# Kernel tuning notes

Measured on AMD Instinct MI355X. Metric: run time of the kernel, lower is better.

The kernel has to match this reference:

```python
import jax, jax.numpy as jnp
import numpy as np

B, S, D, H = 4, 2048, 1024, 16
DH = D // H  # head dim = 64
MASK_VALUE = -1000000.0


def setup_inputs() -> dict:
    key = jax.random.key(0)
    ks = jax.random.split(key, 8)
    return {
        "key": jax.random.normal(ks[0], (B, S, D), jnp.float32),
        "query": jax.random.normal(ks[1], (B, S, D), jnp.float32),
        "value": jax.random.normal(ks[2], (B, S, D), jnp.float32),
        "valid_lens": jax.random.randint(ks[3], (B,), 0, 2048, jnp.int32),
        # nn.Linear weights stored as [out_features, in_features]
        "Wk": jax.random.normal(ks[4], (D, D), jnp.float32) / np.sqrt(D),
        "Wq": jax.random.normal(ks[5], (D, D), jnp.float32) / np.sqrt(D),
        "Wv": jax.random.normal(ks[6], (D, D), jnp.float32) / np.sqrt(D),
        "Wo": jax.random.normal(ks[7], (D, D), jnp.float32) / np.sqrt(D),
    }


def _split_heads(x):
    # [B, S, D] -> [B, H, S, DH]
    return x.reshape(B, S, H, DH).transpose(0, 2, 1, 3)


def reference(key, query, value, valid_lens, Wk, Wq, Wv, Wo):
    # projections (Linear: x @ W^T, bias=False)
    q = _split_heads(query @ Wq.T)  # [B, H, S, DH]
    k = _split_heads(key @ Wk.T)
    v = _split_heads(value @ Wv.T)

    scale = 1.0 / jnp.sqrt(jnp.asarray(DH, q.dtype))
    scores = jnp.einsum("bhqd,bhkd->bhqk", q, k) * scale  # [B, H, S, S]

    # valid_lens masks the key axis per batch element (same for all heads/queries)
    key_mask = jnp.arange(S) < valid_lens[:, None]  # [B, S]
    scores = jnp.where(key_mask[:, None, None, :], scores, MASK_VALUE)

    attn = jax.nn.softmax(scores, axis=-1)
    out = jnp.einsum("bhqk,bhkd->bhqd", attn, v)  # [B, H, S, DH]
    out = out.transpose(0, 2, 1, 3).reshape(B, S, D)  # concat heads
    return out @ Wo.T
```

## Files before the change

### kernel.cpp

```cpp
#include <hip/hip_runtime.h>
#include <hip/hip_bf16.h>
#include <stdint.h>

typedef __bf16 bf16;
typedef __bf16 bf16x4 __attribute__((ext_vector_type(4)));
typedef __bf16 bf16x8 __attribute__((ext_vector_type(8)));
typedef float f32x4 __attribute__((ext_vector_type(4)));
typedef float f32x8 __attribute__((ext_vector_type(8)));

#define MFMA16 __builtin_amdgcn_mfma_f32_16x16x32_bf16

__device__ __forceinline__ void gload_lds16(void* lds, const void* g) {
  __builtin_amdgcn_global_load_lds(
      (const __attribute__((address_space(1))) unsigned int*)g,
      (__attribute__((address_space(3))) unsigned int*)lds, 16, 0, 0);
}

#define S_BARRIER() __builtin_amdgcn_s_barrier()
#define WAIT_LGKM0()                                   \
  do {                                                 \
    asm volatile("s_waitcnt lgkmcnt(0)" ::: "memory"); \
    __builtin_amdgcn_sched_barrier(0);                 \
  } while (0)
#define WAIT_VM(n) asm volatile("s_waitcnt vmcnt(" #n ")" ::: "memory")

__global__ __launch_bounds__(256) void cvt3(
    const float* __restrict__ s0, const float* __restrict__ s1,
    const float* __restrict__ s2, bf16* __restrict__ d0,
    bf16* __restrict__ d1, bf16* __restrict__ d2) {
  const float* srcs[3] = {s0, s1, s2};
  bf16* dsts[3] = {d0, d1, d2};
  const float* src = srcs[blockIdx.y];
  bf16* dst = dsts[blockIdx.y];
  int i = (blockIdx.x * 256 + threadIdx.x) * 4;
  f32x4 v = *(const f32x4*)(src + i);
  bf16x4 o;
#pragma unroll
  for (int j = 0; j < 4; j++) o[j] = (bf16)v[j];
  *(bf16x4*)(dst + i) = o;
}

__global__ __launch_bounds__(256) void cvt1(const float* __restrict__ src,
                                            bf16* __restrict__ dst) {
  int i = (blockIdx.x * 256 + threadIdx.x) * 4;
  f32x4 v = *(const f32x4*)(src + i);
  bf16x4 o;
#pragma unroll
  for (int j = 0; j < 4; j++) o[j] = (bf16)v[j];
  *(bf16x4*)(dst + i) = o;
}

__global__ __launch_bounds__(256) void cvt4(const float* __restrict__ w0,
                                            const float* __restrict__ w1,
                                            const float* __restrict__ w2,
                                            const float* __restrict__ w3,
                                            bf16* __restrict__ dst) {
  const float* srcs[4] = {w0, w1, w2, w3};
  const float* src = srcs[blockIdx.y];
  int i = (blockIdx.x * 256 + threadIdx.x) * 4;
  f32x4 v = *(const f32x4*)(src + i);
  bf16x4 o;
#pragma unroll
  for (int j = 0; j < 4; j++) o[j] = (bf16)v[j];
  *(bf16x4*)(dst + (size_t)blockIdx.y * 1048576 + i) = o;
}

__device__ __forceinline__ void gemmF_body(const bf16* __restrict__ A,
                                           const bf16* __restrict__ W,
                                           void* __restrict__ Craw, int mode,
                                           int m0, int n0, bf16* smem) {
  constexpr int K = 1024;
  const int t = threadIdx.x;
  const int lane = t & 63;
  const int m16 = lane & 15;
  const int quad = (lane >> 4) & 3;
  const int sw = m16 & 7;
  const int w = t >> 6;
  const int wm = (w >> 2) * 64;
  const int wn = (w & 3) * 64;

  const bf16* Ab = A + (size_t)m0 * K;
  const bf16* Bb = W + (size_t)n0 * K;

  auto STG = [&](int buf, int kt) {
    bf16* dA = smem + buf * 24576;
    bf16* dB = dA + 8192;
    const bf16* sA = Ab + kt * 64;
    const bf16* sB = Bb + kt * 64;
#pragma unroll
    for (int ld = 0; ld < 2; ld++) {
      int idx = ld * 512 + t;
      int row = idx >> 3;
      int c = (idx & 7) ^ (row & 7);
      gload_lds16(dA + idx * 8, sA + (size_t)row * K + c * 8);
    }
#pragma unroll
    for (int ld = 0; ld < 4; ld++) {
      int idx = ld * 512 + t;
      int row = idx >> 3;
      int c = (idx & 7) ^ (row & 7);
      gload_lds16(dB + idx * 8, sB + (size_t)row * K + c * 8);
    }
  };

  bf16x8 aR[8], bR[8];
  auto LD = [&](int buf) {
    const bf16* As = smem + buf * 24576;
    const bf16* Bs = As + 8192;
#pragma unroll
    for (int f = 0; f < 4; f++)
#pragma unroll
      for (int ks = 0; ks < 2; ks++) {
        aR[f * 2 + ks] = *(const bf16x8*)&As[(wm + f * 16 + m16) * 64 +
                                             (((ks * 4 + quad) ^ sw) * 8)];
        bR[f * 2 + ks] = *(const bf16x8*)&Bs[(wn + f * 16 + m16) * 64 +
                                             (((ks * 4 + quad) ^ sw) * 8)];
      }
  };

  f32x4 acc[4][4];
#pragma unroll
  for (int f = 0; f < 4; f++)
#pragma unroll
    for (int g = 0; g < 4; g++) acc[f][g] = (f32x4){0.f, 0.f, 0.f, 0.f};

  auto MM = [&]() {
    __builtin_amdgcn_s_setprio(1);
#pragma unroll
    for (int f = 0; f < 4; f++)
#pragma unroll
      for (int g = 0; g < 4; g++)
#pragma unroll
        for (int ks = 0; ks < 2; ks++)
          acc[f][g] = MFMA16(aR[f * 2 + ks], bR[g * 2 + ks], acc[f][g], 0, 0, 0);
    __builtin_amdgcn_s_setprio(0);
  };

  STG(0, 0);
  STG(1, 1);
  WAIT_VM(6);
  S_BARRIER();

  int bufR = 0;
#pragma unroll 1
  for (int kt = 0; kt < 14; ++kt) {
    LD(bufR);
    int bufS = bufR + 2;
    if (bufS >= 3) bufS -= 3;
    STG(bufS, kt + 2);
    S_BARRIER();
    WAIT_LGKM0();
    MM();
    WAIT_VM(6);
    S_BARRIER();
    bufR = (bufR + 1 == 3) ? 0 : bufR + 1;
  }
  LD(bufR);
  S_BARRIER();
  WAIT_LGKM0();
  MM();
  WAIT_VM(0);
  S_BARRIER();
  bufR = (bufR + 1 == 3) ? 0 : bufR + 1;
  LD(bufR);
  S_BARRIER();
  WAIT_LGKM0();
  MM();

#pragma unroll
  for (int f = 0; f < 4; f++) {
    int rbase = m0 + wm + f * 16 + quad * 4;
#pragma unroll
    for (int g = 0; g < 4; g++) {
      int col = n0 + wn + g * 16 + m16;
#pragma unroll
      for (int r = 0; r < 4; r++) {
        int row = rbase + r;
        if (mode == 0) {
          ((float*)Craw)[(size_t)row * 1024 + col] = acc[f][g][r];
        } else {
          int b = row >> 11, s = row & 2047;
          int h = col >> 6, d = col & 63;
          bf16 v = (bf16)acc[f][g][r];
          if (mode == 1)
            ((bf16*)Craw)[(((size_t)(b * 16 + h)) * 2048 + s) * 64 + d] = v;
          else
            ((bf16*)Craw)[(((size_t)(b * 16 + h)) * 64 + d) * 2048 + s] = v;
        }
      }
    }
  }
}

__global__ __launch_bounds__(512, 2) void gemm_qkv(
    const bf16* __restrict__ xq, const bf16* __restrict__ xk,
    const bf16* __restrict__ xv, const bf16* __restrict__ wb,
    const int* __restrict__ vlen, bf16* __restrict__ qp,
    bf16* __restrict__ kp, bf16* __restrict__ vt) {
  __shared__ bf16 smem[73728];
  const int m0 = blockIdx.y * 128;
  const int n0 = blockIdx.x * 256;
  const int z = blockIdx.z;
  if (z >= 1) {
    int b = m0 >> 11;
    int s0 = m0 & 2047;
    int vl = vlen[b];
    if (vl != 0 && s0 >= vl) return;
  }
  const bf16* A = (z == 0) ? xq : (z == 1) ? xk : xv;
  const bf16* W = wb + (size_t)z * 1048576;
  bf16* C = (z == 0) ? qp : (z == 1) ? kp : vt;
  gemmF_body(A, W, C, (z == 2) ? 2 : 1, m0, n0, smem);
}

__global__ __launch_bounds__(512, 2) void gemm_one(const bf16* __restrict__ A,
                                                   const bf16* __restrict__ W,
                                                   void* __restrict__ Craw,
                                                   int mode) {
  __shared__ bf16 smem[73728];
  gemmF_body(A, W, Craw, mode, blockIdx.y * 128, blockIdx.x * 256, smem);
}

template <int AF32, int WF32>
__global__ __launch_bounds__(256) void gemm_bt(const void* __restrict__ Araw,
                                               const void* __restrict__ Wraw,
                                               void* __restrict__ Craw,
                                               int mode) {
  constexpr int K = 1024;
  __shared__ bf16 As[128 * 32];
  __shared__ bf16 Bs[128 * 32];
  const int t = threadIdx.x;
  const int lane = t & 63;
  const int quad = lane >> 4;
  const int m16 = lane & 15;
  const int w = t >> 6;
  const int m0 = blockIdx.y * 128;
  const int n0 = blockIdx.x * 128;
  const int wm = (w >> 1) * 64;
  const int wn = (w & 1) * 64;

  f32x4 acc[4][4];
#pragma unroll
  for (int i = 0; i < 4; i++)
#pragma unroll
    for (int j = 0; j < 4; j++) acc[i][j] = (f32x4){0.f, 0.f, 0.f, 0.f};

  for (int kt = 0; kt < K / 32; kt++) {
    bf16x8 aR[2], bR[2];
#pragma unroll
    for (int p = 0; p < 2; p++) {
      int idx = p * 256 + t;
      int row = idx >> 2;
      int ce = (idx & 3) * 8;
      size_t aoff = (size_t)(m0 + row) * K + kt * 32 + ce;
      size_t boff = (size_t)(n0 + row) * K + kt * 32 + ce;
      if constexpr (AF32) {
        f32x8 av = *(const f32x8*)((const float*)Araw + aoff);
#pragma unroll
        for (int j = 0; j < 8; j++) aR[p][j] = (bf16)av[j];
      } else {
        aR[p] = *(const bf16x8*)((const bf16*)Araw + aoff);
      }
      if constexpr (WF32) {
        f32x8 bv = *(const f32x8*)((const float*)Wraw + boff);
#pragma unroll
        for (int j = 0; j < 8; j++) bR[p][j] = (bf16)bv[j];
      } else {
        bR[p] = *(const bf16x8*)((const bf16*)Wraw + boff);
      }
    }
    __syncthreads();
#pragma unroll
    for (int p = 0; p < 2; p++) {
      int idx = p * 256 + t;
      *(bf16x8*)&As[idx * 8] = aR[p];
      *(bf16x8*)&Bs[idx * 8] = bR[p];
    }
    __syncthreads();

    bf16x8 af[4], bfr[4];
#pragma unroll
    for (int i = 0; i < 4; i++) {
      af[i] = *(const bf16x8*)&As[(wm + i * 16 + m16) * 32 + quad * 8];
      bfr[i] = *(const bf16x8*)&Bs[(wn + i * 16 + m16) * 32 + quad * 8];
    }
#pragma unroll
    for (int i = 0; i < 4; i++)
#pragma unroll
      for (int j = 0; j < 4; j++)
        acc[i][j] = MFMA16(af[i], bfr[j], acc[i][j], 0, 0, 0);
  }

#pragma unroll
  for (int i = 0; i < 4; i++) {
    int rbase = m0 + wm + i * 16 + quad * 4;
#pragma unroll
    for (int j = 0; j < 4; j++) {
      int col = n0 + wn + j * 16 + m16;
#pragma unroll
      for (int r = 0; r < 4; r++) {
        int row = rbase + r;
        if (mode == 0) {
          ((float*)Craw)[(size_t)row * 1024 + col] = acc[i][j][r];
        } else {
          int b = row >> 11, s = row & 2047;
          int h = col >> 6, d = col & 63;
          bf16 v = (bf16)acc[i][j][r];
          if (mode == 1)
            ((bf16*)Craw)[(((size_t)(b * 16 + h)) * 2048 + s) * 64 + d] = v;
          else
            ((bf16*)Craw)[(((size_t)(b * 16 + h)) * 64 + d) * 2048 + s] = v;
        }
      }
    }
  }
}

__global__ __launch_bounds__(256) void attn(const bf16* __restrict__ qp,
                                            const bf16* __restrict__ kp,
                                            const bf16* __restrict__ vt,
                                            const int* __restrict__ vlen,
                                            bf16* __restrict__ ctx) {
  __shared__ bf16 Ks[64 * 64];
  __shared__ bf16 Vs[64 * 64];
  __shared__ bf16 Ps[4 * 32 * 72];

  const int t = threadIdx.x;
  const int lane = t & 63;
  const int quad = lane >> 4;
  const int m16 = lane & 15;
  const int sw = m16 & 7;
  const int w = t >> 6;
  const int bh = blockIdx.y;
  const int qt = blockIdx.x;
  const int b = bh >> 4;
  const int h = bh & 15;
  const int vl = vlen[b];

  const float C1 = 0.18033688f;
  const float C2 = 46.166241f;
  const float mArg = (vl == 0) ? 0.0f : -12800.0f;

  bf16x8 qf[2][2];
#pragma unroll
  for (int a = 0; a < 2; a++) {
    const bf16* qb =
        qp + ((size_t)(bh * 2048 + qt * 128 + w * 32 + a * 16 + m16)) * 64;
    qf[a][0] = *(const bf16x8*)(qb + quad * 8);
    qf[a][1] = *(const bf16x8*)(qb + 32 + quad * 8);
  }

  float rsum[2][4] = {{0.f, 0.f, 0.f, 0.f}, {0.f, 0.f, 0.f, 0.f}};
  f32x4 o[2][4];
#pragma unroll
  for (int a = 0; a < 2; a++)
#pragma unroll
    for (int nt = 0; nt < 4; nt++) o[a][nt] = (f32x4){0.f, 0.f, 0.f, 0.f};

  const int ktEnd = (vl == 0) ? 32 : ((vl + 63) >> 6);

  for (int kt = 0; kt < ktEnd; kt++) {
    __syncthreads();
#pragma unroll
    for (int p = 0; p < 2; p++) {
      int idx = p * 256 + t;
      int row = idx >> 3;
      int gc = (idx & 7) ^ (row & 7);
      gload_lds16(&Ks[idx * 8],
                  &kp[((size_t)(bh * 2048 + kt * 64 + row)) * 64 + gc * 8]);
      gload_lds16(&Vs[idx * 8],
                  &vt[((size_t)(bh * 64 + row)) * 2048 + kt * 64 + gc * 8]);
    }
    __syncthreads();

    f32x4 s[2][4];
#pragma unroll
    for (int a = 0; a < 2; a++)
#pragma unroll
      for (int nt = 0; nt < 4; nt++) s[a][nt] = (f32x4){0.f, 0.f, 0.f, 0.f};
#pragma unroll
    for (int nt = 0; nt < 4; nt++) {
      int key = nt * 16 + m16;
#pragma unroll
      for (int ks = 0; ks < 2; ks++) {
        bf16x8 kf =
            *(const bf16x8*)&Ks[key * 64 + (((ks * 4 + quad) ^ sw) * 8)];
        s[0][nt] = MFMA16(qf[0][ks], kf, s[0][nt], 0, 0, 0);
        s[1][nt] = MFMA16(qf[1][ks], kf, s[1][nt], 0, 0, 0);
      }
    }

#pragma unroll
    for (int nt = 0; nt < 4; nt++) {
      bool masked = (kt * 64 + nt * 16 + m16) >= vl;
#pragma unroll
      for (int a = 0; a < 2; a++)
#pragma unroll
        for (int r = 0; r < 4; r++) {
          float arg = masked ? mArg : (s[a][nt][r] * C1 - C2);
          bf16 pb = (bf16)__builtin_amdgcn_exp2f(arg);
          rsum[a][r] += (float)pb;
          Ps[w * 2304 + (a * 16 + quad * 4 + r) * 72 + nt * 16 + m16] = pb;
        }
    }

#pragma unroll
    for (int ks = 0; ks < 2; ks++) {
      bf16x8 pf0 = *(const bf16x8*)&Ps[w * 2304 + m16 * 72 + ks * 32 + quad * 8];
      bf16x8 pf1 =
          *(const bf16x8*)&Ps[w * 2304 + (16 + m16) * 72 + ks * 32 + quad * 8];
#pragma unroll
      for (int nt = 0; nt < 4; nt++) {
        int dh = nt * 16 + m16;
        bf16x8 vf =
            *(const bf16x8*)&Vs[dh * 64 + (((ks * 4 + quad) ^ sw) * 8)];
        o[0][nt] = MFMA16(pf0, vf, o[0][nt], 0, 0, 0);
        o[1][nt] = MFMA16(pf1, vf, o[1][nt], 0, 0, 0);
      }
    }
  }

#pragma unroll
  for (int off = 1; off < 16; off <<= 1)
#pragma unroll
    for (int a = 0; a < 2; a++)
#pragma unroll
      for (int r = 0; r < 4; r++) rsum[a][r] += __shfl_xor(rsum[a][r], off);
#pragma unroll
  for (int a = 0; a < 2; a++)
#pragma unroll
    for (int r = 0; r < 4; r++) rsum[a][r] = 1.0f / rsum[a][r];

#pragma unroll
  for (int a = 0; a < 2; a++)
#pragma unroll
    for (int nt = 0; nt < 4; nt++) {
      int dh = nt * 16 + m16;
#pragma unroll
      for (int r = 0; r < 4; r++) {
        int srow = qt * 128 + w * 32 + a * 16 + quad * 4 + r;
        ctx[((size_t)(b * 2048 + srow)) * 1024 + h * 64 + dh] =
            (bf16)(o[a][nt][r] * rsum[a][r]);
      }
    }
}

extern "C" void kernel_launch(void* const* d_in, const int* in_sizes, int n_in,
                              void* d_out, int out_size, void* d_ws,
                              size_t ws_size, hipStream_t stream) {
  const float* key = (const float*)d_in[0];
  const float* query = (const float*)d_in[1];
  const float* value = (const float*)d_in[2];
  const int* vlen = (const int*)d_in[3];
  const float* Wk = (const float*)d_in[4];
  const float* Wq = (const float*)d_in[5];
  const float* Wv = (const float*)d_in[6];
  const float* Wo = (const float*)d_in[7];

  const size_t NE = (size_t)4 * 2048 * 1024;
  const size_t WE = 1048576;

  const size_t needA = (6 * NE + 4 * WE) * sizeof(bf16);
  const size_t needB = (5 * NE + 4 * WE) * sizeof(bf16);
  dim3 gg(4, 64), gb(512), cb(256);

  if (ws_size >= needA) {
    bf16* qp = (bf16*)d_ws;
    bf16* kp = qp + NE;
    bf16* vt = kp + NE;
    bf16* xq = vt + NE;
    bf16* xk = xq + NE;
    bf16* xv = xk + NE;
    bf16* wb = xv + NE;
    bf16* ctx = xq;

    cvt4<<<dim3(1024, 4), cb, 0, stream>>>(Wq, Wk, Wv, Wo, wb);
    cvt3<<<dim3(8192, 3), cb, 0, stream>>>(query, key, value, xq, xk, xv);
    gemm_qkv<<<dim3(4, 64, 3), gb, 0, stream>>>(xq, xk, xv, wb, vlen, qp, kp,
                                                vt);
    attn<<<dim3(16, 64), cb, 0, stream>>>(qp, kp, vt, vlen, ctx);
    gemm_one<<<gg, gb, 0, stream>>>(ctx, wb + 3 * WE, d_out, 0);
  } else if (ws_size >= needB) {
    bf16* qp = (bf16*)d_ws;
    bf16* kp = qp + NE;
    bf16* vt = kp + NE;
    bf16* ctx = vt + NE;
    bf16* xb = ctx + NE;
    bf16* wb = xb + NE;

    cvt4<<<dim3(1024, 4), cb, 0, stream>>>(Wq, Wk, Wv, Wo, wb);
    cvt1<<<8192, cb, 0, stream>>>(query, xb);
    gemm_one<<<gg, gb, 0, stream>>>(xb, wb + 0 * WE, qp, 1);
    cvt1<<<8192, cb, 0, stream>>>(key, xb);
    gemm_one<<<gg, gb, 0, stream>>>(xb, wb + 1 * WE, kp, 1);
    cvt1<<<8192, cb, 0, stream>>>(value, xb);
    gemm_one<<<gg, gb, 0, stream>>>(xb, wb + 2 * WE, vt, 2);
    attn<<<dim3(16, 64), cb, 0, stream>>>(qp, kp, vt, vlen, ctx);
    gemm_one<<<gg, gb, 0, stream>>>(ctx, wb + 3 * WE, d_out, 0);
  } else {
    bf16* qp = (bf16*)d_ws;
    bf16* kp = qp + NE;
    bf16* vt = kp + NE;
    bf16* ctx = vt + NE;
    dim3 g8(8, 64), b256(256);
    gemm_bt<1, 1><<<g8, b256, 0, stream>>>(query, Wq, qp, 1);
    gemm_bt<1, 1><<<g8, b256, 0, stream>>>(key, Wk, kp, 1);
    gemm_bt<1, 1><<<g8, b256, 0, stream>>>(value, Wv, vt, 2);
    attn<<<dim3(16, 64), b256, 0, stream>>>(qp, kp, vt, vlen, ctx);
    gemm_bt<0, 1><<<g8, b256, 0, stream>>>(ctx, Wo, d_out, 0);
  }
}
```

Before: 320.7 us.

## Double-buffer K/V tiles in attention with 512-thread blocks and XCD-aware mapping

The attention kernel now uses 512-thread blocks covering 256 queries, so each staged K/V tile is reused by twice as many warps. K/V tiles are double-buffered in LDS, with the next tile's async global-to-LDS load issued before computing on the current one, and waits use vmcnt plus raw barriers. Block IDs are remapped so that query tiles of the same head land on the same XCD for L2 reuse. The cost is more LDS per block and fewer blocks in flight, and the raw barrier and vmcnt synchronisation is easy to get wrong.

```diff
diff --git a/kernel.cpp b/kernel.cpp
--- a/kernel.cpp
+++ b/kernel.cpp
@@ -316,23 +316,26 @@
   }
 }
 
-__global__ __launch_bounds__(256) void attn(const bf16* __restrict__ qp,
-                                            const bf16* __restrict__ kp,
-                                            const bf16* __restrict__ vt,
-                                            const int* __restrict__ vlen,
-                                            bf16* __restrict__ ctx) {
-  __shared__ bf16 Ks[64 * 64];
-  __shared__ bf16 Vs[64 * 64];
-  __shared__ bf16 Ps[4 * 32 * 72];
+__global__ __launch_bounds__(512, 4) void attn(const bf16* __restrict__ qp,
+                                               const bf16* __restrict__ kp,
+                                               const bf16* __restrict__ vt,
+                                               const int* __restrict__ vlen,
+                                               bf16* __restrict__ ctx) {
+  __shared__ bf16 Ks[2][4096];
+  __shared__ bf16 Vs[2][4096];
+  __shared__ bf16 Ps[8 * 2304];
 
   const int t = threadIdx.x;
   const int lane = t & 63;
-  const int quad = lane >> 4;
+  const int quad = (lane >> 4) & 3;
   const int m16 = lane & 15;
   const int sw = m16 & 7;
   const int w = t >> 6;
-  const int bh = blockIdx.y;
-  const int qt = blockIdx.x;
+  const int id = blockIdx.y * 8 + blockIdx.x;
+  const int xcd = id & 7;
+  const int j = id >> 3;
+  const int bh = (j >> 3) * 8 + xcd;
+  const int qt = j & 7;
   const int b = bh >> 4;
   const int h = bh & 15;
   const int vl = vlen[b];
@@ -345,7 +348,7 @@
 #pragma unroll
   for (int a = 0; a < 2; a++) {
     const bf16* qb =
-        qp + ((size_t)(bh * 2048 + qt * 128 + w * 32 + a * 16 + m16)) * 64;
+        qp + ((size_t)(bh * 2048 + qt * 256 + w * 32 + a * 16 + m16)) * 64;
     qf[a][0] = *(const bf16x8*)(qb + quad * 8);
     qf[a][1] = *(const bf16x8*)(qb + 32 + quad * 8);
   }
@@ -359,19 +362,28 @@
 
   const int ktEnd = (vl == 0) ? 32 : ((vl + 63) >> 6);
 
+  const int srow = t >> 3;
+  const int sgc = (t & 7) ^ (srow & 7);
+  auto STAGE = [&](int buf, int kt) {
+    gload_lds16(&Ks[buf][t * 8],
+                &kp[((size_t)(bh * 2048 + kt * 64 + srow)) * 64 + sgc * 8]);
+    gload_lds16(&Vs[buf][t * 8],
+                &vt[((size_t)(bh * 64 + srow)) * 2048 + kt * 64 + sgc * 8]);
+  };
+
+  STAGE(0, 0);
+
   for (int kt = 0; kt < ktEnd; kt++) {
-    __syncthreads();
-#pragma unroll
-    for (int p = 0; p < 2; p++) {
-      int idx = p * 256 + t;
-      int row = idx >> 3;
-      int gc = (idx & 7) ^ (row & 7);
-      gload_lds16(&Ks[idx * 8],
-                  &kp[((size_t)(bh * 2048 + kt * 64 + row)) * 64 + gc * 8]);
-      gload_lds16(&Vs[idx * 8],
-                  &vt[((size_t)(bh * 64 + row)) * 2048 + kt * 64 + gc * 8]);
-    }
-    __syncthreads();
+    const int cur = kt & 1;
+    if (kt + 1 < ktEnd) {
+      STAGE(cur ^ 1, kt + 1);
+      WAIT_VM(2);
+    } else {
+      WAIT_VM(0);
+    }
+    S_BARRIER();
+    const bf16* Ksb = Ks[cur];
+    const bf16* Vsb = Vs[cur];
 
     f32x4 s[2][4];
 #pragma unroll
@@ -384,7 +396,7 @@
 #pragma unroll
       for (int ks = 0; ks < 2; ks++) {
         bf16x8 kf =
-            *(const bf16x8*)&Ks[key * 64 + (((ks * 4 + quad) ^ sw) * 8)];
+            *(const bf16x8*)&Ksb[key * 64 + (((ks * 4 + quad) ^ sw) * 8)];
         s[0][nt] = MFMA16(qf[0][ks], kf, s[0][nt], 0, 0, 0);
         s[1][nt] = MFMA16(qf[1][ks], kf, s[1][nt], 0, 0, 0);
       }
@@ -413,11 +425,12 @@
       for (int nt = 0; nt < 4; nt++) {
         int dh = nt * 16 + m16;
         bf16x8 vf =
-            *(const bf16x8*)&Vs[dh * 64 + (((ks * 4 + quad) ^ sw) * 8)];
+            *(const bf16x8*)&Vsb[dh * 64 + (((ks * 4 + quad) ^ sw) * 8)];
         o[0][nt] = MFMA16(pf0, vf, o[0][nt], 0, 0, 0);
         o[1][nt] = MFMA16(pf1, vf, o[1][nt], 0, 0, 0);
       }
     }
+    S_BARRIER();
   }
 
 #pragma unroll
@@ -438,8 +451,8 @@
       int dh = nt * 16 + m16;
 #pragma unroll
       for (int r = 0; r < 4; r++) {
-        int srow = qt * 128 + w * 32 + a * 16 + quad * 4 + r;
-        ctx[((size_t)(b * 2048 + srow)) * 1024 + h * 64 + dh] =
+        int sr = qt * 256 + w * 32 + a * 16 + quad * 4 + r;
+        ctx[((size_t)(b * 2048 + sr)) * 1024 + h * 64 + dh] =
             (bf16)(o[a][nt][r] * rsum[a][r]);
       }
     }
@@ -462,7 +475,7 @@
 
   const size_t needA = (6 * NE + 4 * WE) * sizeof(bf16);
   const size_t needB = (5 * NE + 4 * WE) * sizeof(bf16);
-  dim3 gg(4, 64), gb(512), cb(256);
+  dim3 gg(4, 64), gb(512), cb(256), ag(8, 64), ab(512);
 
   if (ws_size >= needA) {
     bf16* qp = (bf16*)d_ws;
@@ -478,7 +491,7 @@
     cvt3<<<dim3(8192, 3), cb, 0, stream>>>(query, key, value, xq, xk, xv);
     gemm_qkv<<<dim3(4, 64, 3), gb, 0, stream>>>(xq, xk, xv, wb, vlen, qp, kp,
                                                 vt);
-    attn<<<dim3(16, 64), cb, 0, stream>>>(qp, kp, vt, vlen, ctx);
+    attn<<<ag, ab, 0, stream>>>(qp, kp, vt, vlen, ctx);
     gemm_one<<<gg, gb, 0, stream>>>(ctx, wb + 3 * WE, d_out, 0);
   } else if (ws_size >= needB) {
     bf16* qp = (bf16*)d_ws;
@@ -495,7 +508,7 @@
     gemm_one<<<gg, gb, 0, stream>>>(xb, wb + 1 * WE, kp, 1);
     cvt1<<<8192, cb, 0, stream>>>(value, xb);
     gemm_one<<<gg, gb, 0, stream>>>(xb, wb + 2 * WE, vt, 2);
-    attn<<<dim3(16, 64), cb, 0, stream>>>(qp, kp, vt, vlen, ctx);
+    attn<<<ag, ab, 0, stream>>>(qp, kp, vt, vlen, ctx);
     gemm_one<<<gg, gb, 0, stream>>>(ctx, wb + 3 * WE, d_out, 0);
   } else {
     bf16* qp = (bf16*)d_ws;
@@ -506,7 +519,7 @@
     gemm_bt<1, 1><<<g8, b256, 0, stream>>>(query, Wq, qp, 1);
     gemm_bt<1, 1><<<g8, b256, 0, stream>>>(key, Wk, kp, 1);
     gemm_bt<1, 1><<<g8, b256, 0, stream>>>(value, Wv, vt, 2);
-    attn<<<dim3(16, 64), b256, 0, stream>>>(qp, kp, vt, vlen, ctx);
+    attn<<<ag, ab, 0, stream>>>(qp, kp, vt, vlen, ctx);
     gemm_bt<0, 1><<<g8, b256, 0, stream>>>(ctx, Wo, d_out, 0);
   }
 }
```

Result: slower. 328.7 us (+2.5%).
